# Kernel optimization log

Hardware: AMD Instinct MI355X
Metric: run time of the kernel (lower is better)

## Reference

```python
import jax, jax.numpy as jnp
import numpy as np

EMBED_DIM = 512
NUM_HEADS = 8
HEAD_DIM = EMBED_DIM // NUM_HEADS
SCALING = HEAD_DIM ** -0.5
T, B = 2048, 4
NEG_INF = -1e9


def setup_inputs() -> dict:
    key = jax.random.key(0)
    k1, k2, k3 = jax.random.split(key, 3)
    h = jax.random.normal(k1, (T, B, EMBED_DIM), dtype=jnp.float32)
    # causal additive mask, [T, T]: 0 on/below diagonal, -inf above
    attn_mask = jnp.where(jnp.triu(jnp.ones((T, T), dtype=bool), k=1), NEG_INF, 0.0).astype(jnp.float32)
    in_proj_weight = jax.random.normal(k2, (3 * EMBED_DIM, EMBED_DIM), dtype=jnp.float32) * 0.02
    in_proj_bias = jnp.zeros((3 * EMBED_DIM,), dtype=jnp.float32)
    out_w = jax.random.normal(k3, (EMBED_DIM, EMBED_DIM), dtype=jnp.float32) * 0.02
    out_b = jnp.zeros((EMBED_DIM,), dtype=jnp.float32)
    return {"h": h, "attn_mask": attn_mask, "in_proj_weight": in_proj_weight,
            "in_proj_bias": in_proj_bias, "out_w": out_w, "out_b": out_b}


def reference(h, attn_mask, in_proj_weight, in_proj_bias, out_w, out_b):
    tgt_len, bsz, embed_dim = h.shape
    # fused QKV projection: [T, B, 3E]
    qkv = jnp.einsum('tbe,fe->tbf', h, in_proj_weight) + in_proj_bias
    q, k, v = jnp.split(qkv, 3, axis=-1)
    q = q * SCALING
    # [T, B, E] -> [B*H, T, hd]
    def to_heads(x):
        return x.reshape(tgt_len, bsz * NUM_HEADS, HEAD_DIM).transpose(1, 0, 2)
    q, k, v = to_heads(q), to_heads(k), to_heads(v)
    # scores: [B*H, T, S]
    attn_weights = jnp.einsum('bth,bsh->bts', q, k)
    attn_weights = attn_weights + attn_mask[None, :, :]
    attn_p = jax.nn.softmax(attn_weights, axis=-1)
    attn = jnp.einsum('bts,bsh->bth', attn_p, v)
    # [B*H, T, hd] -> [T, B, E]
    attn = attn.transpose(1, 0, 2).reshape(tgt_len, bsz, embed_dim)
    out = jnp.einsum('tbe,fe->tbf', attn, out_w) + out_b
    return out, attn_p.reshape(bsz, NUM_HEADS, tgt_len, tgt_len)
```

## Files before the change

kernel.cpp:

```cpp
#include <hip/hip_runtime.h>
#include <cstdint>
#include <cstddef>

#define T_SEQ 2048
#define BSZ 4
#define EMB 512
#define NH 8
#define HD 64
#define SCALING 0.125f
#define NEGBIG (-1e30f)
#define KVB 128
#define PW 136

typedef short bf16x8_t __attribute__((ext_vector_type(8)));
typedef float f32x4_t __attribute__((ext_vector_type(4)));
typedef short short4v __attribute__((ext_vector_type(4)));
typedef float float4v __attribute__((ext_vector_type(4)));

typedef __attribute__((address_space(1))) const void* as1_cvp;
typedef __attribute__((address_space(3))) void* as3_vp;

#define MFMA16(a, b, c) __builtin_amdgcn_mfma_f32_16x16x32_bf16((a), (b), (c), 0, 0, 0)

static __device__ __forceinline__ short f2b(float f) {
  union { float f; uint32_t u; } x; x.f = f;
  uint32_t r = (x.u + 0x7fffu + ((x.u >> 16) & 1u)) >> 16;
  return (short)(r & 0xffffu);
}

static __device__ __forceinline__ void gload_lds16(const void* g, void* l) {
  __builtin_amdgcn_global_load_lds((as1_cvp)g, (as3_vp)l, 16, 0, 0);
}

__global__ __launch_bounds__(256) void cvt_kernel(const float* __restrict__ in,
                                                  short* __restrict__ out) {
  int i = (blockIdx.x * 256 + threadIdx.x) * 4;
  float4v v = *(const float4v*)(in + i);
  short4v o;
  o[0] = f2b(v[0]); o[1] = f2b(v[1]); o[2] = f2b(v[2]); o[3] = f2b(v[3]);
  *(short4v*)(out + i) = o;
}

template <int EPI>
__global__ __launch_bounds__(256)
void gemm_bt(const short* __restrict__ A, const short* __restrict__ Bt,
             const float* __restrict__ bias,
             short* __restrict__ outQ, short* __restrict__ outK, short* __restrict__ outV,
             float* __restrict__ outF) {
  __shared__ short ldsA[128 * 32];
  __shared__ short ldsB[128 * 32];
  const int tid = threadIdx.x;
  const int wid = tid >> 6, lane = tid & 63, g = lane >> 4, r16 = lane & 15;
  const int wr = wid >> 1, wc = wid & 1;
  const int mbase = blockIdx.y * 128, nbase = blockIdx.x * 128;

  f32x4_t acc[4][4];
#pragma unroll
  for (int m = 0; m < 4; ++m)
#pragma unroll
    for (int n = 0; n < 4; ++n) acc[m][n] = (f32x4_t){0.f, 0.f, 0.f, 0.f};

  for (int kt = 0; kt < 16; ++kt) {
    __syncthreads();
#pragma unroll
    for (int i = 0; i < 2; ++i) {
      int c = i * 256 + tid;
      int row = c >> 2, j4 = c & 3;
      gload_lds16(A + (size_t)(mbase + row) * 512 + kt * 32 + j4 * 8, &ldsA[c * 8]);
      gload_lds16(Bt + (size_t)(nbase + row) * 512 + kt * 32 + j4 * 8, &ldsB[c * 8]);
    }
    __syncthreads();
    bf16x8_t af[4], bfv[4];
#pragma unroll
    for (int m = 0; m < 4; ++m)
      af[m] = *(const bf16x8_t*)&ldsA[(wr * 64 + m * 16 + r16) * 32 + g * 8];
#pragma unroll
    for (int n = 0; n < 4; ++n)
      bfv[n] = *(const bf16x8_t*)&ldsB[(wc * 64 + n * 16 + r16) * 32 + g * 8];
#pragma unroll
    for (int m = 0; m < 4; ++m)
#pragma unroll
      for (int n = 0; n < 4; ++n) acc[m][n] = MFMA16(af[m], bfv[n], acc[m][n]);
  }

#pragma unroll
  for (int m = 0; m < 4; ++m) {
#pragma unroll
    for (int n = 0; n < 4; ++n) {
      int col = nbase + wc * 64 + n * 16 + r16;
      float bcol = bias[col];
#pragma unroll
      for (int j = 0; j < 4; ++j) {
        int row = mbase + wr * 64 + m * 16 + g * 4 + j;
        float v = acc[m][n][j] + bcol;
        if (EPI == 0) {
          int sect = col >> 9, e = col & 511, hh = e >> 6, d = e & 63;
          int t = row >> 2, b = row & 3;
          size_t dst = ((size_t)(b * NH + hh) * T_SEQ + t) * HD + d;
          short bv = f2b(v);
          if (sect == 0) outQ[dst] = bv;
          else if (sect == 1) outK[dst] = bv;
          else outV[dst] = bv;
        } else {
          outF[(size_t)row * EMB + col] = v;
        }
      }
    }
  }
}

__global__ __launch_bounds__(256)
void attn_fused(const short* __restrict__ Qg, const short* __restrict__ Kg,
                const short* __restrict__ Vg, float* __restrict__ Pout,
                short* __restrict__ attnO) {
  __shared__ short Kt[KVB * 64];
  __shared__ short Vt[64 * PW];
  __shared__ short Pl[4][16 * PW];
  const int bh = blockIdx.x;
  const int qt = 31 - (int)blockIdx.y;
  const int tid = threadIdx.x, wid = tid >> 6, lane = tid & 63;
  const int g = lane >> 4, r16 = lane & 15;
  const size_t headOff = (size_t)bh * T_SEQ * HD;
  const int wrow0 = qt * 64 + wid * 16;
  const int maxcol = qt * 64 + 64;
  const int nkt = (qt >> 1) + 1;

  bf16x8_t qf[2];
  {
    const short* qp = Qg + headOff + (size_t)(wrow0 + r16) * HD + g * 8;
    qf[0] = *(const bf16x8_t*)qp;
    qf[1] = *(const bf16x8_t*)(qp + 32);
  }

  float m1 = NEGBIG, l1 = 0.f;
  const int myrow = wrow0 + r16;
  for (int kt = 0; kt < nkt; ++kt) {
    const int kb = kt * KVB;
    const int navail = (maxcol - kb) >> 4;
    const int nkc = navail < 8 ? navail : 8;
    __syncthreads();
#pragma unroll
    for (int i = 0; i < 4; ++i) {
      int c = i * 256 + tid;
      int row = c >> 3, j8 = (c & 7) ^ (row & 7);
      gload_lds16(Kg + headOff + (size_t)(kb + row) * HD + j8 * 8, &Kt[c * 8]);
    }
    __syncthreads();
    float sv[8][4];
#pragma unroll
    for (int kc = 0; kc < 8; ++kc) {
      if (kc < nkc) {
        f32x4_t s = {0.f, 0.f, 0.f, 0.f};
        const int rl = kc * 16 + r16;
#pragma unroll
        for (int kk = 0; kk < 2; ++kk) {
          int byteo = (rl * 128 + kk * 64 + g * 16) ^ ((rl & 7) << 4);
          bf16x8_t kf = *(const bf16x8_t*)((const char*)Kt + byteo);
          s = MFMA16(kf, qf[kk], s);
        }
        const bool nomask = (kb + kc * 16 + 15 <= wrow0);
#pragma unroll
        for (int j = 0; j < 4; ++j) {
          int key = kb + kc * 16 + g * 4 + j;
          float v = s[j] * SCALING;
          sv[kc][j] = (nomask || key <= myrow) ? v : NEGBIG;
        }
      }
    }
    float pm = NEGBIG;
#pragma unroll
    for (int kc = 0; kc < 8; ++kc)
      if (kc < nkc) {
#pragma unroll
        for (int j = 0; j < 4; ++j) pm = fmaxf(pm, sv[kc][j]);
      }
    float mn = fmaxf(m1, pm);
    float sum = 0.f;
#pragma unroll
    for (int kc = 0; kc < 8; ++kc)
      if (kc < nkc) {
#pragma unroll
        for (int j = 0; j < 4; ++j) sum += __expf(sv[kc][j] - mn);
      }
    l1 = l1 * __expf(m1 - mn) + sum;
    m1 = mn;
  }
#pragma unroll
  for (int off = 16; off <= 32; off <<= 1) {
    float mo = __shfl_xor(m1, off), lo = __shfl_xor(l1, off);
    float mn = fmaxf(m1, mo);
    l1 = l1 * __expf(m1 - mn) + lo * __expf(mo - mn);
    m1 = mn;
  }
  float m2[4], rl2[4];
  int trow[4];
#pragma unroll
  for (int j = 0; j < 4; ++j) {
    m2[j] = __shfl(m1, g * 4 + j);
    rl2[j] = 1.0f / __shfl(l1, g * 4 + j);
    trow[j] = wrow0 + g * 4 + j;
  }

  f32x4_t oacc[4];
#pragma unroll
  for (int dc = 0; dc < 4; ++dc) oacc[dc] = (f32x4_t){0.f, 0.f, 0.f, 0.f};

  uint32_t* Vtu = (uint32_t*)Vt;
  for (int kt = 0; kt < nkt; ++kt) {
    const int kb = kt * KVB;
    const int navail = (maxcol - kb) >> 4;
    const int nkc = navail < 8 ? navail : 8;
    __syncthreads();
#pragma unroll
    for (int i = 0; i < 4; ++i) {
      int c = i * 256 + tid;
      int row = c >> 3, j8 = (c & 7) ^ (row & 7);
      gload_lds16(Kg + headOff + (size_t)(kb + row) * HD + j8 * 8, &Kt[c * 8]);
    }
#pragma unroll
    for (int i = 0; i < 2; ++i) {
      int c = i * 256 + tid;
      int kp = c & 63, dg = c >> 6;
      const short* vp = Vg + headOff + (size_t)(kb + kp * 2) * HD + dg * 8;
      bf16x8_t va = *(const bf16x8_t*)vp;
      bf16x8_t vb = *(const bf16x8_t*)(vp + HD);
#pragma unroll
      for (int j = 0; j < 8; ++j)
        Vtu[(dg * 8 + j) * (PW / 2) + kp] =
            (uint32_t)(uint16_t)va[j] | ((uint32_t)(uint16_t)vb[j] << 16);
    }
    __syncthreads();
#pragma unroll
    for (int kc = 0; kc < 8; ++kc) {
      if (kc < nkc) {
        f32x4_t s = {0.f, 0.f, 0.f, 0.f};
        const int rl = kc * 16 + r16;
#pragma unroll
        for (int kk = 0; kk < 2; ++kk) {
          int byteo = (rl * 128 + kk * 64 + g * 16) ^ ((rl & 7) << 4);
          bf16x8_t kf = *(const bf16x8_t*)((const char*)Kt + byteo);
          s = MFMA16(qf[kk], kf, s);
        }
        int col = kb + kc * 16 + r16;
#pragma unroll
        for (int j = 0; j < 4; ++j) {
          float e = __expf(s[j] * SCALING - m2[j]) * rl2[j];
          float pv = (col <= trow[j]) ? e : 0.f;
          Pout[((size_t)bh * T_SEQ + trow[j]) * T_SEQ + col] = pv;
          Pl[wid][(g * 4 + j) * PW + kc * 16 + r16] = f2b(pv);
        }
      }
    }
#pragma unroll
    for (int kc2 = 0; kc2 < 4; ++kc2) {
      if (kc2 < (nkc >> 1)) {
        bf16x8_t pf = *(const bf16x8_t*)&Pl[wid][r16 * PW + kc2 * 32 + g * 8];
#pragma unroll
        for (int dc = 0; dc < 4; ++dc) {
          bf16x8_t vf = *(const bf16x8_t*)&Vt[(dc * 16 + r16) * PW + kc2 * 32 + g * 8];
          oacc[dc] = MFMA16(pf, vf, oacc[dc]);
        }
      }
    }
  }

#pragma unroll
  for (int dc = 0; dc < 4; ++dc) {
#pragma unroll
    for (int j = 0; j < 4; ++j) {
      int t = trow[j], d = dc * 16 + r16;
      size_t ntok = (size_t)t * BSZ + (bh >> 3);
      attnO[ntok * EMB + (bh & 7) * HD + d] = f2b(oacc[dc][j]);
    }
  }

  const int c0 = maxcol;
  const int nc4 = (T_SEQ - c0) >> 2;
  for (int r = 0; r < 64; ++r) {
    size_t base = ((size_t)bh * T_SEQ + qt * 64 + r) * T_SEQ + c0;
    for (int c4 = tid; c4 < nc4; c4 += 256) {
      float4v z = {0.f, 0.f, 0.f, 0.f};
      *(float4v*)(Pout + base + (size_t)c4 * 4) = z;
    }
  }
}

extern "C" void kernel_launch(void* const* d_in, const int* in_sizes, int n_in,
                              void* d_out, int out_size, void* d_ws, size_t ws_size,
                              hipStream_t stream) {
  const float* h = (const float*)d_in[0];
  const float* w_in = (const float*)d_in[2];
  const float* b_in = (const float*)d_in[3];
  const float* w_out = (const float*)d_in[4];
  const float* b_out = (const float*)d_in[5];
  float* out = (float*)d_out;
  float* Pout = out + (size_t)T_SEQ * BSZ * EMB;

  short* hB = (short*)d_ws;
  short* wB = hB + (size_t)8192 * 512;
  short* owB = wB + (size_t)1536 * 512;
  short* qB = owB + (size_t)512 * 512;
  short* kB = qB + (size_t)32 * 2048 * 64;
  short* vB = kB + (size_t)32 * 2048 * 64;
  short* aB = vB + (size_t)32 * 2048 * 64;

  cvt_kernel<<<4096, 256, 0, stream>>>(h, hB);
  cvt_kernel<<<768, 256, 0, stream>>>(w_in, wB);
  cvt_kernel<<<256, 256, 0, stream>>>(w_out, owB);

  gemm_bt<0><<<dim3(12, 64), 256, 0, stream>>>(hB, wB, b_in, qB, kB, vB, nullptr);
  attn_fused<<<dim3(32, 32), 256, 0, stream>>>(qB, kB, vB, Pout, aB);
  gemm_bt<1><<<dim3(4, 64), 256, 0, stream>>>(aB, owB, b_out, nullptr, nullptr, nullptr, out);
}
```

Measured before the change: 230.6 us.

## Split attention over two KV halves with separate stats, PV, and reduction kernels

The fused attention kernel becomes three kernels. A stats kernel computes partial softmax max/sum for each half of the key range, a PV kernel recombines the two stats and writes probabilities plus partial outputs per half, and a small kernel sums the halves and converts to bf16. This doubles the grid so more blocks run in parallel and long causal rows are balanced better. It also writes P as float4 along rows with a transposed score MFMA and widens the LDS pitch, at the cost of extra launches and an fp32 partial-output round trip through global memory.

```diff
diff --git a/kernel.cpp b/kernel.cpp
--- a/kernel.cpp
+++ b/kernel.cpp
@@ -10,7 +10,7 @@
 #define SCALING 0.125f
 #define NEGBIG (-1e30f)
 #define KVB 128
-#define PW 136
+#define PW 144
 
 typedef short bf16x8_t __attribute__((ext_vector_type(8)));
 typedef float f32x4_t __attribute__((ext_vector_type(4)));
@@ -110,40 +110,45 @@
 }
 
 __global__ __launch_bounds__(256)
-void attn_fused(const short* __restrict__ Qg, const short* __restrict__ Kg,
-                const short* __restrict__ Vg, float* __restrict__ Pout,
-                short* __restrict__ attnO) {
+void attn_stats(const short* __restrict__ Qg, const short* __restrict__ Kg,
+                float2* __restrict__ stats) {
   __shared__ short Kt[KVB * 64];
-  __shared__ short Vt[64 * PW];
-  __shared__ short Pl[4][16 * PW];
-  const int bh = blockIdx.x;
-  const int qt = 31 - (int)blockIdx.y;
+  const int bh = blockIdx.x, c = blockIdx.y;
+  const int qt = 31 - (int)blockIdx.z;
   const int tid = threadIdx.x, wid = tid >> 6, lane = tid & 63;
   const int g = lane >> 4, r16 = lane & 15;
   const size_t headOff = (size_t)bh * T_SEQ * HD;
   const int wrow0 = qt * 64 + wid * 16;
   const int maxcol = qt * 64 + 64;
   const int nkt = (qt >> 1) + 1;
+  const int hsp = (nkt + 1) >> 1;
+  const int t0 = c ? hsp : 0, t1 = c ? nkt : hsp;
+  const int myrow = wrow0 + r16;
+  float2* srow = stats + (size_t)(bh * 2 + c) * T_SEQ;
+
+  if (t0 >= t1) {
+    if (g == 0) srow[myrow] = make_float2(NEGBIG, 0.f);
+    return;
+  }
 
   bf16x8_t qf[2];
   {
-    const short* qp = Qg + headOff + (size_t)(wrow0 + r16) * HD + g * 8;
+    const short* qp = Qg + headOff + (size_t)myrow * HD + g * 8;
     qf[0] = *(const bf16x8_t*)qp;
     qf[1] = *(const bf16x8_t*)(qp + 32);
   }
 
   float m1 = NEGBIG, l1 = 0.f;
-  const int myrow = wrow0 + r16;
-  for (int kt = 0; kt < nkt; ++kt) {
+  for (int kt = t0; kt < t1; ++kt) {
     const int kb = kt * KVB;
     const int navail = (maxcol - kb) >> 4;
     const int nkc = navail < 8 ? navail : 8;
     __syncthreads();
 #pragma unroll
     for (int i = 0; i < 4; ++i) {
-      int c = i * 256 + tid;
-      int row = c >> 3, j8 = (c & 7) ^ (row & 7);
-      gload_lds16(Kg + headOff + (size_t)(kb + row) * HD + j8 * 8, &Kt[c * 8]);
+      int cc = i * 256 + tid;
+      int row = cc >> 3, j8 = (cc & 7) ^ (row & 7);
+      gload_lds16(Kg + headOff + (size_t)(kb + row) * HD + j8 * 8, &Kt[cc * 8]);
     }
     __syncthreads();
     float sv[8][4];
@@ -162,8 +167,7 @@
 #pragma unroll
         for (int j = 0; j < 4; ++j) {
           int key = kb + kc * 16 + g * 4 + j;
-          float v = s[j] * SCALING;
-          sv[kc][j] = (nomask || key <= myrow) ? v : NEGBIG;
+          sv[kc][j] = (nomask || key <= myrow) ? s[j] * SCALING : NEGBIG;
         }
       }
     }
@@ -192,97 +196,142 @@
     l1 = l1 * __expf(m1 - mn) + lo * __expf(mo - mn);
     m1 = mn;
   }
-  float m2[4], rl2[4];
-  int trow[4];
-#pragma unroll
-  for (int j = 0; j < 4; ++j) {
-    m2[j] = __shfl(m1, g * 4 + j);
-    rl2[j] = 1.0f / __shfl(l1, g * 4 + j);
-    trow[j] = wrow0 + g * 4 + j;
-  }
+  if (g == 0) srow[myrow] = make_float2(m1, l1);
+}
+
+__global__ __launch_bounds__(256)
+void attn_pw(const short* __restrict__ Qg, const short* __restrict__ Kg,
+             const short* __restrict__ Vg, const float2* __restrict__ stats,
+             float* __restrict__ Pout, float* __restrict__ Opart) {
+  __shared__ short Kt[KVB * 64];
+  __shared__ short Vt[64 * PW];
+  __shared__ short Pl[4][16 * PW];
+  const int bh = blockIdx.x, c = blockIdx.y;
+  const int qt = 31 - (int)blockIdx.z;
+  const int tid = threadIdx.x, wid = tid >> 6, lane = tid & 63;
+  const int g = lane >> 4, r16 = lane & 15;
+  const size_t headOff = (size_t)bh * T_SEQ * HD;
+  const int wrow0 = qt * 64 + wid * 16;
+  const int maxcol = qt * 64 + 64;
+  const int nkt = (qt >> 1) + 1;
+  const int hsp = (nkt + 1) >> 1;
+  const int t0 = c ? hsp : 0, t1 = c ? nkt : hsp;
+  const int myrow = wrow0 + r16;
+
+  float2 s0 = stats[(size_t)(bh * 2 + 0) * T_SEQ + myrow];
+  float2 s1 = stats[(size_t)(bh * 2 + 1) * T_SEQ + myrow];
+  float mfin = fmaxf(s0.x, s1.x);
+  float lfin = s0.y * __expf(s0.x - mfin) + s1.y * __expf(s1.x - mfin);
+  float rl2 = 1.0f / lfin;
 
   f32x4_t oacc[4];
 #pragma unroll
   for (int dc = 0; dc < 4; ++dc) oacc[dc] = (f32x4_t){0.f, 0.f, 0.f, 0.f};
 
-  uint32_t* Vtu = (uint32_t*)Vt;
-  for (int kt = 0; kt < nkt; ++kt) {
-    const int kb = kt * KVB;
-    const int navail = (maxcol - kb) >> 4;
-    const int nkc = navail < 8 ? navail : 8;
-    __syncthreads();
-#pragma unroll
-    for (int i = 0; i < 4; ++i) {
-      int c = i * 256 + tid;
-      int row = c >> 3, j8 = (c & 7) ^ (row & 7);
-      gload_lds16(Kg + headOff + (size_t)(kb + row) * HD + j8 * 8, &Kt[c * 8]);
-    }
-#pragma unroll
-    for (int i = 0; i < 2; ++i) {
-      int c = i * 256 + tid;
-      int kp = c & 63, dg = c >> 6;
-      const short* vp = Vg + headOff + (size_t)(kb + kp * 2) * HD + dg * 8;
-      bf16x8_t va = *(const bf16x8_t*)vp;
-      bf16x8_t vb = *(const bf16x8_t*)(vp + HD);
-#pragma unroll
-      for (int j = 0; j < 8; ++j)
-        Vtu[(dg * 8 + j) * (PW / 2) + kp] =
-            (uint32_t)(uint16_t)va[j] | ((uint32_t)(uint16_t)vb[j] << 16);
-    }
-    __syncthreads();
-#pragma unroll
-    for (int kc = 0; kc < 8; ++kc) {
-      if (kc < nkc) {
-        f32x4_t s = {0.f, 0.f, 0.f, 0.f};
-        const int rl = kc * 16 + r16;
-#pragma unroll
-        for (int kk = 0; kk < 2; ++kk) {
-          int byteo = (rl * 128 + kk * 64 + g * 16) ^ ((rl & 7) << 4);
-          bf16x8_t kf = *(const bf16x8_t*)((const char*)Kt + byteo);
-          s = MFMA16(qf[kk], kf, s);
-        }
-        int col = kb + kc * 16 + r16;
-#pragma unroll
-        for (int j = 0; j < 4; ++j) {
-          float e = __expf(s[j] * SCALING - m2[j]) * rl2[j];
-          float pv = (col <= trow[j]) ? e : 0.f;
-          Pout[((size_t)bh * T_SEQ + trow[j]) * T_SEQ + col] = pv;
-          Pl[wid][(g * 4 + j) * PW + kc * 16 + r16] = f2b(pv);
-        }
-      }
-    }
-#pragma unroll
-    for (int kc2 = 0; kc2 < 4; ++kc2) {
-      if (kc2 < (nkc >> 1)) {
-        bf16x8_t pf = *(const bf16x8_t*)&Pl[wid][r16 * PW + kc2 * 32 + g * 8];
-#pragma unroll
-        for (int dc = 0; dc < 4; ++dc) {
-          bf16x8_t vf = *(const bf16x8_t*)&Vt[(dc * 16 + r16) * PW + kc2 * 32 + g * 8];
-          oacc[dc] = MFMA16(pf, vf, oacc[dc]);
-        }
-      }
-    }
-  }
-
+  if (t0 < t1) {
+    bf16x8_t qf[2];
+    {
+      const short* qp = Qg + headOff + (size_t)myrow * HD + g * 8;
+      qf[0] = *(const bf16x8_t*)qp;
+      qf[1] = *(const bf16x8_t*)(qp + 32);
+    }
+    uint32_t* Vtu = (uint32_t*)Vt;
+    for (int kt = t0; kt < t1; ++kt) {
+      const int kb = kt * KVB;
+      const int navail = (maxcol - kb) >> 4;
+      const int nkc = navail < 8 ? navail : 8;
+      __syncthreads();
+#pragma unroll
+      for (int i = 0; i < 4; ++i) {
+        int cc = i * 256 + tid;
+        int row = cc >> 3, j8 = (cc & 7) ^ (row & 7);
+        gload_lds16(Kg + headOff + (size_t)(kb + row) * HD + j8 * 8, &Kt[cc * 8]);
+      }
+#pragma unroll
+      for (int i = 0; i < 2; ++i) {
+        int cc = i * 256 + tid;
+        int kp = cc & 63, dg = cc >> 6;
+        const short* vp = Vg + headOff + (size_t)(kb + kp * 2) * HD + dg * 8;
+        bf16x8_t va = *(const bf16x8_t*)vp;
+        bf16x8_t vb = *(const bf16x8_t*)(vp + HD);
+#pragma unroll
+        for (int j = 0; j < 8; ++j)
+          Vtu[(dg * 8 + j) * (PW / 2) + kp] =
+              (uint32_t)(uint16_t)va[j] | ((uint32_t)(uint16_t)vb[j] << 16);
+      }
+      __syncthreads();
+#pragma unroll
+      for (int kc = 0; kc < 8; ++kc) {
+        if (kc < nkc) {
+          f32x4_t s = {0.f, 0.f, 0.f, 0.f};
+          const int rl = kc * 16 + r16;
+#pragma unroll
+          for (int kk = 0; kk < 2; ++kk) {
+            int byteo = (rl * 128 + kk * 64 + g * 16) ^ ((rl & 7) << 4);
+            bf16x8_t kf = *(const bf16x8_t*)((const char*)Kt + byteo);
+            s = MFMA16(kf, qf[kk], s);
+          }
+          const int key0 = kb + kc * 16 + g * 4;
+          float4v pvv;
+          short4v pb;
+#pragma unroll
+          for (int j = 0; j < 4; ++j) {
+            float e = __expf(s[j] * SCALING - mfin) * rl2;
+            pvv[j] = (key0 + j <= myrow) ? e : 0.f;
+            pb[j] = f2b(pvv[j]);
+          }
+          *(float4v*)(Pout + ((size_t)bh * T_SEQ + myrow) * T_SEQ + key0) = pvv;
+          *(short4v*)&Pl[wid][r16 * PW + kc * 16 + g * 4] = pb;
+        }
+      }
+#pragma unroll
+      for (int kc2 = 0; kc2 < 4; ++kc2) {
+        if (kc2 < (nkc >> 1)) {
+          bf16x8_t pf = *(const bf16x8_t*)&Pl[wid][r16 * PW + kc2 * 32 + g * 8];
+#pragma unroll
+          for (int dc = 0; dc < 4; ++dc) {
+            bf16x8_t vf = *(const bf16x8_t*)&Vt[(dc * 16 + r16) * PW + kc2 * 32 + g * 8];
+            oacc[dc] = MFMA16(pf, vf, oacc[dc]);
+          }
+        }
+      }
+    }
+  }
+
+  float* orow = Opart + (size_t)(c * 32 + bh) * T_SEQ * HD;
 #pragma unroll
   for (int dc = 0; dc < 4; ++dc) {
 #pragma unroll
-    for (int j = 0; j < 4; ++j) {
-      int t = trow[j], d = dc * 16 + r16;
-      size_t ntok = (size_t)t * BSZ + (bh >> 3);
-      attnO[ntok * EMB + (bh & 7) * HD + d] = f2b(oacc[dc][j]);
-    }
-  }
-
-  const int c0 = maxcol;
-  const int nc4 = (T_SEQ - c0) >> 2;
-  for (int r = 0; r < 64; ++r) {
-    size_t base = ((size_t)bh * T_SEQ + qt * 64 + r) * T_SEQ + c0;
-    for (int c4 = tid; c4 < nc4; c4 += 256) {
-      float4v z = {0.f, 0.f, 0.f, 0.f};
-      *(float4v*)(Pout + base + (size_t)c4 * 4) = z;
-    }
-  }
+    for (int j = 0; j < 4; ++j)
+      orow[(size_t)(wrow0 + g * 4 + j) * HD + dc * 16 + r16] = oacc[dc][j];
+  }
+
+  if (c == 1) {
+    const int c0 = maxcol;
+    const int nc4 = (T_SEQ - c0) >> 2;
+    for (int r = 0; r < 64; ++r) {
+      size_t base = ((size_t)bh * T_SEQ + qt * 64 + r) * T_SEQ + c0;
+      for (int c4 = tid; c4 < nc4; c4 += 256) {
+        float4v z = {0.f, 0.f, 0.f, 0.f};
+        *(float4v*)(Pout + base + (size_t)c4 * 4) = z;
+      }
+    }
+  }
+}
+
+__global__ __launch_bounds__(256)
+void osum_cvt(const float* __restrict__ Opart, short* __restrict__ aB) {
+  int i = (blockIdx.x * 256 + threadIdx.x) * 4;
+  int tok = i >> 9, e = i & 511;
+  int b = tok & 3, t = tok >> 2, hh = e >> 6, d = e & 63;
+  int bh = b * NH + hh;
+  size_t o = ((size_t)bh * T_SEQ + t) * HD + d;
+  float4v a = *(const float4v*)(Opart + o);
+  float4v b4 = *(const float4v*)(Opart + (size_t)32 * T_SEQ * HD + o);
+  short4v r;
+#pragma unroll
+  for (int j = 0; j < 4; ++j) r[j] = f2b(a[j] + b4[j]);
+  *(short4v*)(aB + (size_t)tok * EMB + e) = r;
 }
 
 extern "C" void kernel_launch(void* const* d_in, const int* in_sizes, int n_in,
@@ -303,12 +352,16 @@
   short* kB = qB + (size_t)32 * 2048 * 64;
   short* vB = kB + (size_t)32 * 2048 * 64;
   short* aB = vB + (size_t)32 * 2048 * 64;
+  float2* stats = (float2*)(aB + (size_t)8192 * 512);
+  float* Opart = (float*)(stats + (size_t)32 * 2 * T_SEQ);
 
   cvt_kernel<<<4096, 256, 0, stream>>>(h, hB);
   cvt_kernel<<<768, 256, 0, stream>>>(w_in, wB);
   cvt_kernel<<<256, 256, 0, stream>>>(w_out, owB);
 
   gemm_bt<0><<<dim3(12, 64), 256, 0, stream>>>(hB, wB, b_in, qB, kB, vB, nullptr);
-  attn_fused<<<dim3(32, 32), 256, 0, stream>>>(qB, kB, vB, Pout, aB);
+  attn_stats<<<dim3(32, 2, 32), 256, 0, stream>>>(qB, kB, stats);
+  attn_pw<<<dim3(32, 2, 32), 256, 0, stream>>>(qB, kB, vB, stats, Pout, Opart);
+  osum_cvt<<<4096, 256, 0, stream>>>(Opart, aB);
   gemm_bt<1><<<dim3(4, 64), 256, 0, stream>>>(aB, owB, b_out, nullptr, nullptr, nullptr, out);
 }
```

New measurement: 233.1 us. Within noise of the previous version (+1.1%).
